# Optimization experiments

Measured on AMD Instinct MI355X. Metric: run time of the kernel, lower is better.

The kernel has to match this reference:

```python
import jax, jax.numpy as jnp
import numpy as np

KS = 32        # kernel_size (chunk size)
STRIDE = 16    # kernel_stride
H = 8          # head_num_k
D = 128        # head_dim
B = 4          # number of sequences
SEQ = 8192     # tokens per sequence (equal-length varlen batch)


def setup_inputs() -> dict:
    key = jax.random.key(0)
    k1, k2, k3, k4, k5 = jax.random.split(key, 5)
    kv = jax.random.normal(k1, (B * SEQ, 2, H, D), dtype=jnp.float32)
    cu_seqlens = jnp.arange(B + 1, dtype=jnp.int32) * SEQ
    # torch Conv1d default init: uniform(-s, s), s = 1/sqrt(in_channels*kernel_size)
    s = 1.0 / np.sqrt(D * KS)
    k_conv_w = jax.random.uniform(k2, (D, D, KS), jnp.float32, -s, s)
    k_conv_b = jax.random.uniform(k3, (D,), jnp.float32, -s, s)
    v_conv_w = jax.random.uniform(k4, (D, D, KS), jnp.float32, -s, s)
    v_conv_b = jax.random.uniform(k5, (D,), jnp.float32, -s, s)
    return {"kv": kv, "cu_seqlens": cu_seqlens,
            "k_conv_w": k_conv_w, "k_conv_b": k_conv_b,
            "v_conv_w": v_conv_w, "v_conv_b": v_conv_b}


def _chunk_indices(cu_seqlens, total_tokens):
    # Equal-length sequences: every strided chunk is valid, so shapes are static.
    batch = cu_seqlens.shape[0] - 1
    seqlen = total_tokens // batch
    nc = (seqlen - KS) // STRIDE + 1  # chunks per sequence
    starts = cu_seqlens[:-1].astype(jnp.int32)          # [B]
    offs = (jnp.arange(nc, dtype=jnp.int32) * STRIDE)   # [nc]
    pos = jnp.arange(KS, dtype=jnp.int32)               # [KS]
    idx = starts[:, None, None] + offs[None, :, None] + pos[None, None, :]  # [B, nc, KS]
    cu_comp = jnp.arange(batch + 1, dtype=jnp.int32) * nc
    return idx.reshape(batch * nc, KS), cu_comp


def reference(kv, cu_seqlens, k_conv_w, k_conv_b, v_conv_w, v_conv_b):
    idx, cu_comp = _chunk_indices(cu_seqlens, kv.shape[0])  # [L, KS]
    filtered = kv[idx.reshape(-1)].reshape(idx.shape[0], KS, 2, H, D)  # [L, KS, 2, H, D]
    k = filtered[:, :, 0]  # [L, KS, H, D]
    v = filtered[:, :, 1]
    # Conv1d with kernel spanning the whole chunk -> single output position:
    # out[l,h,o] = sum_{i,t} x[l,t,h,i] * W[o,i,t] + b[o]
    compress_k = jnp.einsum('lthi,oit->lho', k, k_conv_w) + k_conv_b
    compress_v = jnp.einsum('lthi,oit->lho', v, v_conv_w) + v_conv_b
    return compress_k, compress_v, cu_comp
```

## Files before the change

### kernel.cpp

```cpp
#include <hip/hip_runtime.h>

typedef __attribute__((ext_vector_type(8))) short bf16x8;
typedef __attribute__((ext_vector_type(4))) float f32x4;

#define MFMA16(A, B, C) __builtin_amdgcn_mfma_f32_16x16x32_bf16(A, B, C, 0, 0, 0)

__device__ __forceinline__ unsigned short f2bf(float f) {
  union { float f; unsigned int u; } v; v.f = f;
  return (unsigned short)((v.u + 0x7fffu + ((v.u >> 16) & 1u)) >> 16);
}
#define PK(LO, HI) (((unsigned int)f2bf(LO)) | ((unsigned int)f2bf(HI) << 16))

#define BAR() do {                                              \
    asm volatile("s_waitcnt lgkmcnt(0)" ::: "memory");          \
    __builtin_amdgcn_s_barrier();                               \
    asm volatile("" ::: "memory");                              \
  } while (0)

__global__ __launch_bounds__(256) void prep_kernel(
    const float* __restrict__ kw, const float* __restrict__ vw,
    unsigned short* __restrict__ imgK, unsigned short* __restrict__ imgV,
    int KSd,
    const int* __restrict__ cuin, float* __restrict__ outf,
    int cubase, int nb, int strideh) {
  __shared__ float wlds[128 * 33];
  int tid = threadIdx.x, bid = blockIdx.x;
  int sel = bid >> 7, o = bid & 127;
  int nel = 128 * KSd;
  int ksh = (KSd == 32) ? 5 : ((KSd == 16) ? 4 : 31 - __clz(KSd));
  int pad = KSd + 1;
  const float* wo = (sel ? vw : kw) + (size_t)o * nel;
  unsigned short* dst = sel ? imgV : imgK;
  for (int idx = tid; idx < nel; idx += 256) {
    int i = idx >> ksh, t = idx & (KSd - 1);
    wlds[i * pad + t] = wo[idx];
  }
  __syncthreads();
  int swE = (o & 7) << 3;
  for (int idx = tid; idx < nel; idx += 256) {
    int s = idx >> 6, c = idx & 63;
    int i = ((s & 1) << 6) + (c ^ swE);
    dst[((size_t)s << 13) + (o << 6) + c] = f2bf(wlds[i * pad + (s >> 1)]);
  }
  if (bid == 0 && tid <= nb) outf[cubase + tid] = (float)(cuin[tid] / strideh);
}

__global__ __launch_bounds__(512) void gemm_breg2_kernel(
    const float* __restrict__ kv,
    const float* __restrict__ biasK, const float* __restrict__ biasV,
    const unsigned short* __restrict__ imgK, const unsigned short* __restrict__ imgV,
    float* __restrict__ out,
    int vbase, int nc, int ltot, int tokmax, int seqb, int mtiles) {
  __shared__ __align__(16) unsigned short T[2][16640];
  int tid = threadIdx.x, bid = blockIdx.x;
  int per_sel = 8 * mtiles;
  int sel = (bid >= per_sel) ? 1 : 0;
  int rem = bid - sel * per_sel;
  int h = rem / mtiles, mtile = rem - h * mtiles;
  int m0 = mtile * 128;
  const unsigned short* img = sel ? imgV : imgK;
  const float* bias = sel ? biasV : biasK;
  int outbase = sel ? vbase : 0;
  int lane = tid & 63, wid = tid >> 6;
  int wm = wid >> 2, wn = wid & 3;
  int l15 = lane & 15, l4 = lane >> 4;

  int b0 = m0 / nc, c0 = m0 - b0 * nc;
  int btok0 = b0 * seqb + c0 * 16;
  int rb = nc - c0;

  int sjl = tid >> 4, sje = tid & 15;
  int soff = sel * 1024 + h * 128 + sje * 8;

  int kb0 = l4 * 16;
  int jbL[4], jswL[4], jbH[4], jswH[4];
#pragma unroll
  for (int mi = 0; mi < 4; ++mi) {
    int r = wm * 64 + mi * 16 + l15;
    int j = r + (r >= rb ? 1 : 0);
    jbL[mi] = j * 256;       jswL[mi] = (j & 7) << 4;
    jbH[mi] = (j + 1) * 256; jswH[mi] = ((j + 1) & 7) << 4;
  }

  int o0 = wn * 32 + l15, o1 = o0 + 16;
  int swE0 = (o0 & 7) << 3, swE1 = (o1 & 7) << 3;
  int ke = l4 * 8;
  int bo00 = o0 * 64 + ((ke) ^ swE0);
  int bo01 = o1 * 64 + ((ke) ^ swE1);
  int bo10 = o0 * 64 + ((32 + ke) ^ swE0);
  int bo11 = o1 * 64 + ((32 + ke) ^ swE1);

  f32x4 zz = {0.f, 0.f, 0.f, 0.f};
  f32x4 acc[4][2];
#pragma unroll
  for (int mi = 0; mi < 4; ++mi) { acc[mi][0] = zz; acc[mi][1] = zz; }

  float4 ta[5], tb[5];
  bf16x8 Bc0, Bc1, Bc2, Bc3, Bn0, Bn1, Bn2, Bn3;

#define STAGE_LOAD(P) do {                                                       \
    _Pragma("unroll")                                                            \
    for (int q_ = 0; q_ < 4; ++q_) {                                             \
      int t_ = btok0 + (q_ * 32 + sjl) * 16 + (P); if (t_ > tokmax) t_ = tokmax; \
      const float* a_ = kv + ((size_t)t_ << 11) + soff;                          \
      ta[q_] = *(const float4*)a_; tb[q_] = *(const float4*)(a_ + 4);            \
    }                                                                            \
    if (sjl < 2) {                                                               \
      int t_ = btok0 + (128 + sjl) * 16 + (P); if (t_ > tokmax) t_ = tokmax;     \
      const float* a_ = kv + ((size_t)t_ << 11) + soff;                          \
      ta[4] = *(const float4*)a_; tb[4] = *(const float4*)(a_ + 4);              \
    }                                                                            \
  } while (0)

#define T_WRITE(TB) do {                                                         \
    char* tp_ = (char*)(TB);                                                     \
    _Pragma("unroll")                                                            \
    for (int q_ = 0; q_ < 4; ++q_) {                                             \
      int js_ = q_ * 32 + sjl;                                                   \
      *(uint4*)(tp_ + js_ * 256 + ((sje * 16) ^ ((js_ & 7) << 4))) =             \
        make_uint4(PK(ta[q_].x, ta[q_].y), PK(ta[q_].z, ta[q_].w),               \
                   PK(tb[q_].x, tb[q_].y), PK(tb[q_].z, tb[q_].w));              \
    }                                                                            \
    if (sjl < 2) {                                                               \
      int js_ = 128 + sjl;                                                       \
      *(uint4*)(tp_ + js_ * 256 + ((sje * 16) ^ ((js_ & 7) << 4))) =             \
        make_uint4(PK(ta[4].x, ta[4].y), PK(ta[4].z, ta[4].w),                   \
                   PK(tb[4].x, tb[4].y), PK(tb[4].z, tb[4].w));                  \
    }                                                                            \
  } while (0)

#define B_LOADR(D0, D1, D2, D3, S) do {                                          \
    const unsigned short* bp_ = img + ((size_t)(S) << 13);                       \
    D0 = *(const bf16x8*)(bp_ + bo00);                                           \
    D1 = *(const bf16x8*)(bp_ + bo01);                                           \
    D2 = *(const bf16x8*)(bp_ + bo10);                                           \
    D3 = *(const bf16x8*)(bp_ + bo11);                                           \
  } while (0)

#define SUBSTEP(HF, JB, JSW, B00, B01, B10, B11) do {                            \
    const char* tc_ = (const char*)T[tcur];                                      \
    __builtin_amdgcn_s_setprio(1);                                               \
    {                                                                            \
      int kcA_ = (HF) * 128 + kb0;                                               \
      bf16x8 a_[4];                                                              \
      _Pragma("unroll")                                                          \
      for (int mi = 0; mi < 4; ++mi)                                             \
        a_[mi] = *(const bf16x8*)(tc_ + JB[mi] + (kcA_ ^ JSW[mi]));              \
      _Pragma("unroll")                                                          \
      for (int mi = 0; mi < 4; ++mi) {                                           \
        acc[mi][0] = MFMA16(a_[mi], B00, acc[mi][0]);                            \
        acc[mi][1] = MFMA16(a_[mi], B01, acc[mi][1]);                            \
      }                                                                          \
    }                                                                            \
    {                                                                            \
      int kcA_ = (HF) * 128 + 64 + kb0;                                          \
      bf16x8 a_[4];                                                              \
      _Pragma("unroll")                                                          \
      for (int mi = 0; mi < 4; ++mi)                                             \
        a_[mi] = *(const bf16x8*)(tc_ + JB[mi] + (kcA_ ^ JSW[mi]));              \
      _Pragma("unroll")                                                          \
      for (int mi = 0; mi < 4; ++mi) {                                           \
        acc[mi][0] = MFMA16(a_[mi], B10, acc[mi][0]);                            \
        acc[mi][1] = MFMA16(a_[mi], B11, acc[mi][1]);                            \
      }                                                                          \
    }                                                                            \
    __builtin_amdgcn_s_setprio(0);                                               \
  } while (0)

  int tcur = 0;
  STAGE_LOAD(0);
  T_WRITE(T[0]);
  B_LOADR(Bc0, Bc1, Bc2, Bc3, 0);
  B_LOADR(Bn0, Bn1, Bn2, Bn3, 1);
  BAR();

  for (int p = 0; p < 16; ++p) {
    if (p < 15) STAGE_LOAD(p + 1);
    SUBSTEP(0, jbL, jswL, Bc0, Bc1, Bc2, Bc3);
    B_LOADR(Bc0, Bc1, Bc2, Bc3, 2 * p + 32);
    SUBSTEP(1, jbL, jswL, Bn0, Bn1, Bn2, Bn3);
    B_LOADR(Bn0, Bn1, Bn2, Bn3, 2 * p + 33);
    SUBSTEP(0, jbH, jswH, Bc0, Bc1, Bc2, Bc3);
    if (p < 15) B_LOADR(Bc0, Bc1, Bc2, Bc3, 2 * p + 2);
    SUBSTEP(1, jbH, jswH, Bn0, Bn1, Bn2, Bn3);
    if (p < 15) {
      B_LOADR(Bn0, Bn1, Bn2, Bn3, 2 * p + 3);
      T_WRITE(T[tcur ^ 1]);
      BAR();
    }
    tcur ^= 1;
  }

#pragma unroll
  for (int ni = 0; ni < 2; ++ni) {
    int o_ = wn * 32 + ni * 16 + l15;
    float bv_ = bias[o_];
#pragma unroll
    for (int mi = 0; mi < 4; ++mi) {
      int lb_ = m0 + wm * 64 + mi * 16 + l4 * 4;
      f32x4 v_ = acc[mi][ni];
#pragma unroll
      for (int jj = 0; jj < 4; ++jj) {
        int ll_ = lb_ + jj;
        if (ll_ < ltot)
          out[(size_t)outbase + (size_t)ll_ * 1024 + h * 128 + o_] = v_[jj] + bv_;
      }
    }
  }
}

__global__ __launch_bounds__(512) void gemm_kernel(
    const float* __restrict__ kv,
    const float* __restrict__ biasK, const float* __restrict__ biasV,
    const unsigned short* __restrict__ imgK, const unsigned short* __restrict__ imgV,
    const float* __restrict__ kw, const float* __restrict__ vw,
    float* __restrict__ out,
    int selbase, int vbase, int nc, int ltot, int nsteps,
    int tokmax, int seqb, int strideh, int KSd, int mtiles) {
  __shared__ __align__(16) unsigned short As[2][4096];
  __shared__ __align__(16) unsigned short Bsf[2][8192];
  int tid = threadIdx.x, bid = blockIdx.x;
  int per_sel = 8 * mtiles;
  int sel = selbase + (bid >= per_sel);
  int rem = (bid >= per_sel) ? bid - per_sel : bid;
  int h = rem / mtiles, mtile = rem - h * mtiles;
  int m0 = mtile * 64;
  const unsigned short* img = sel ? imgV : imgK;
  const float* bias = sel ? biasV : biasK;
  const float* wsel = sel ? vw : kw;
  int outbase = sel ? vbase : 0;
  int lane = tid & 63, wid = tid >> 6;
  int warpM = wid >> 2, warpN = wid & 3;

  int aj = tid & 7, r = tid >> 3;
  int l = m0 + r; if (l > ltot - 1) l = ltot - 1;
  int b = l / nc, c = l - b * nc;
  int btok = b * seqb + c * strideh;
  const float* abase = kv + sel * 1024 + h * 128 + aj * 4;
  int swr = (r & 7) << 3;
  int awb0 = r * 128 + 2 * ((aj * 4) ^ swr);
  int awb1 = r * 128 + 2 * ((aj * 4 + 32) ^ swr);

  int o_g = tid >> 3, cb_g = (tid & 7) << 3;
  int ib_g = cb_g ^ ((o_g & 7) << 3);
  const float* g0 = wsel + (size_t)o_g * (KSd << 7);
  const float* g1 = g0 + ((size_t)64 * (KSd << 7));

  int kb0 = (lane >> 4) * 16;
  int arb[2], asw[2], brb[2], bsw[2];
#pragma unroll
  for (int mi = 0; mi < 2; ++mi) {
    int rr = warpM * 32 + mi * 16 + (lane & 15);
    arb[mi] = rr * 128; asw[mi] = (rr & 7) << 4;
  }
#pragma unroll
  for (int ni = 0; ni < 2; ++ni) {
    int oo = warpN * 32 + ni * 16 + (lane & 15);
    brb[ni] = oo * 128; bsw[ni] = (oo & 7) << 4;
  }

  f32x4 acc[2][2];
  f32x4 zz = {0.f, 0.f, 0.f, 0.f};
#pragma unroll
  for (int a = 0; a < 2; ++a)
#pragma unroll
    for (int b2 = 0; b2 < 2; ++b2) acc[a][b2] = zz;

  float4 Af0, Af1;
  uint4 Brr[2];

#define LOAD_STEP(S) do {                                                        \
    int tok_ = btok + ((S) >> 1); if (tok_ > tokmax) tok_ = tokmax;              \
    const float* ap_ = abase + ((size_t)tok_ << 11) + (((S) & 1) << 6);          \
    Af0 = *(const float4*)ap_;                                                   \
    Af1 = *(const float4*)(ap_ + 32);                                            \
    if (img) {                                                                   \
      const uint4* bsrc_ = (const uint4*)(img + ((size_t)(S) << 13));            \
      Brr[0] = bsrc_[tid];                                                       \
      Brr[1] = bsrc_[512 + tid];                                                 \
    } else {                                                                     \
      int t_ = (S) >> 1, i0_ = (((S) & 1) << 6) + ib_g;                          \
      unsigned int p0_[4], p1_[4];                                               \
      _Pragma("unroll")                                                          \
      for (int m = 0; m < 4; ++m) {                                              \
        p0_[m] = (unsigned int)f2bf(g0[(i0_ + 2*m) * KSd + t_])                  \
               | ((unsigned int)f2bf(g0[(i0_ + 2*m + 1) * KSd + t_]) << 16);     \
        p1_[m] = (unsigned int)f2bf(g1[(i0_ + 2*m) * KSd + t_])                  \
               | ((unsigned int)f2bf(g1[(i0_ + 2*m + 1) * KSd + t_]) << 16);     \
      }                                                                          \
      Brr[0] = make_uint4(p0_[0], p0_[1], p0_[2], p0_[3]);                       \
      Brr[1] = make_uint4(p1_[0], p1_[1], p1_[2], p1_[3]);                       \
    }                                                                            \
  } while (0)

#define WRITE_STEP(DB) do {                                                      \
    *(uint2*)((char*)As[DB] + awb0) = make_uint2(PK(Af0.x, Af0.y), PK(Af0.z, Af0.w)); \
    *(uint2*)((char*)As[DB] + awb1) = make_uint2(PK(Af1.x, Af1.y), PK(Af1.z, Af1.w)); \
    uint4* bdst_ = (uint4*)Bsf[DB];                                              \
    bdst_[tid] = Brr[0];                                                         \
    bdst_[512 + tid] = Brr[1];                                                   \
  } while (0)

#define COMPUTE_STEP(CB) do {                                                    \
    _Pragma("unroll")                                                            \
    for (int kk = 0; kk < 2; ++kk) {                                             \
      bf16x8 af_[2], bg_[2];                                                     \
      int kc_ = kk * 64 + kb0;                                                   \
      _Pragma("unroll")                                                          \
      for (int mi = 0; mi < 2; ++mi)                                             \
        af_[mi] = *(const bf16x8*)((const char*)As[CB] + arb[mi] + (kc_ ^ asw[mi])); \
      _Pragma("unroll")                                                          \
      for (int ni = 0; ni < 2; ++ni)                                             \
        bg_[ni] = *(const bf16x8*)((const char*)Bsf[CB] + brb[ni] + (kc_ ^ bsw[ni])); \
      _Pragma("unroll")                                                          \
      for (int mi = 0; mi < 2; ++mi)                                             \
      _Pragma("unroll")                                                          \
        for (int ni = 0; ni < 2; ++ni)                                           \
          acc[mi][ni] = MFMA16(af_[mi], bg_[ni], acc[mi][ni]);                   \
    }                                                                            \
  } while (0)

  LOAD_STEP(0);
  WRITE_STEP(0);
  __syncthreads();
  int cur = 0;
  for (int s = 0; s < nsteps; ++s) {
    if (s + 1 < nsteps) LOAD_STEP(s + 1);
    COMPUTE_STEP(cur);
    if (s + 1 < nsteps) WRITE_STEP(cur ^ 1);
    __syncthreads();
    cur ^= 1;
  }

  int l15 = lane & 15, l4 = lane >> 4;
#pragma unroll
  for (int ni = 0; ni < 2; ++ni) {
    int o = warpN * 32 + ni * 16 + l15;
    float bv = bias[o];
#pragma unroll
    for (int mi = 0; mi < 2; ++mi) {
      int lb = m0 + warpM * 32 + mi * 16 + l4 * 4;
      f32x4 v = acc[mi][ni];
#pragma unroll
      for (int jj = 0; jj < 4; ++jj) {
        int ll = lb + jj;
        if (ll < ltot)
          out[(size_t)outbase + (size_t)ll * 1024 + h * 128 + o] = v[jj] + bv;
      }
    }
  }
}

extern "C" void kernel_launch(void* const* d_in, const int* in_sizes, int n_in,
                              void* d_out, int out_size, void* d_ws, size_t ws_size,
                              hipStream_t stream) {
  long kvN = 0; int kvi = 0;
  for (int i = 0; i < n_in; ++i)
    if ((long)in_sizes[i] > kvN) { kvN = in_sizes[i]; kvi = i; }
  const float* kv = (const float*)d_in[kvi];
  const float *w0 = nullptr, *w1 = nullptr, *b0 = nullptr, *b1 = nullptr;
  const int* cuin = nullptr;
  int KSd = 32, nb = 4;
  for (int i = 0; i < n_in; ++i) {
    if (i == kvi) continue;
    int sz = in_sizes[i];
    if (sz == 128) { if (!b0) b0 = (const float*)d_in[i]; else if (!b1) b1 = (const float*)d_in[i]; }
    else if (sz <= 32) { nb = sz - 1; cuin = (const int*)d_in[i]; }
    else if (sz >= 4096) {
      if (!w0) { w0 = (const float*)d_in[i]; KSd = sz / 16384; }
      else if (!w1) w1 = (const float*)d_in[i];
    }
  }
  if (!w0) w0 = (const float*)d_in[2];
  if (!b0) b0 = (const float*)d_in[3];
  if (!w1) w1 = (const float*)d_in[4];
  if (!b1) b1 = (const float*)d_in[5];
  if (!cuin) cuin = (const int*)d_in[1];
  if (nb < 1) nb = 4;

  float* out = (float*)d_out;

  int cubase  = out_size - (nb + 1);
  int vbase   = cubase >> 1;
  int ltot    = cubase >> 11;
  int nc      = ltot / nb;
  int nsteps  = 2 * KSd;
  long tokens = kvN >> 11;
  int seqb    = (int)(tokens / nb);
  int strideh = (nc > 1) ? (seqb - KSd) / (nc - 1) : KSd;
  int tokmax  = (int)tokens - 1;
  int mtiles  = (ltot + 63) >> 6;
  int mt128   = (ltot + 127) >> 7;
  int per_sel = 8 * mtiles;

  size_t imgel = (size_t)nsteps * 8192;
  size_t imgbytes = imgel * 2;
  bool fast = (KSd == 32) && (strideh == 16) && (nc >= 128) &&
              (ws_size >= 2 * imgbytes);
  if (fast) {
    unsigned short* imgK = (unsigned short*)d_ws;
    unsigned short* imgV = imgK + imgel;
    prep_kernel<<<256, 256, 0, stream>>>(w0, w1, imgK, imgV, KSd,
                                         cuin, out, cubase, nb, strideh);
    gemm_breg2_kernel<<<2 * 8 * mt128, 512, 0, stream>>>(
        kv, b0, b1, imgK, imgV, out, vbase, nc, ltot, tokmax, seqb, mt128);
  } else if (ws_size >= 2 * imgbytes) {
    unsigned short* imgK = (unsigned short*)d_ws;
    unsigned short* imgV = imgK + imgel;
    prep_kernel<<<256, 256, 0, stream>>>(w0, w1, imgK, imgV, KSd,
                                         cuin, out, cubase, nb, strideh);
    gemm_kernel<<<2 * per_sel, 512, 0, stream>>>(kv, b0, b1, imgK, imgV, w0, w1, out,
        0, vbase, nc, ltot, nsteps, tokmax, seqb, strideh, KSd, mtiles);
  } else {
    prep_kernel<<<256, 256, 0, stream>>>(w0, w1, (unsigned short*)d_ws,
                                         (unsigned short*)d_ws, 0,
                                         cuin, out, cubase, nb, strideh);
    gemm_kernel<<<2 * per_sel, 512, 0, stream>>>(kv, b0, b1,
        (const unsigned short*)nullptr, (const unsigned short*)nullptr, w0, w1, out,
        0, vbase, nc, ltot, nsteps, tokmax, seqb, strideh, KSd, mtiles);
  }
}
```

Before: 79.64 us.

## Split K across warp pairs in fast GEMM and reduce partial sums via LDS

Changes the 8-warp layout from a 2x4 M-by-N grid to a 2x2 grid with two K-halves. Each warp now computes a 64x64 output tile over half of each K slice, so it reads fewer A fragments from LDS per MFMA. The two partial results are summed through shared memory before the bias add and store. This costs more accumulator registers (16 f32x4 instead of 8) and adds a reduction pass with an extra barrier at the end.

```diff
diff --git a/kernel.cpp b/kernel.cpp
--- a/kernel.cpp
+++ b/kernel.cpp
@@ -45,7 +45,7 @@
   if (bid == 0 && tid <= nb) outf[cubase + tid] = (float)(cuin[tid] / strideh);
 }
 
-__global__ __launch_bounds__(512) void gemm_breg2_kernel(
+__global__ __launch_bounds__(512) void gemm_ksplit_kernel(
     const float* __restrict__ kv,
     const float* __restrict__ biasK, const float* __restrict__ biasV,
     const unsigned short* __restrict__ imgK, const unsigned short* __restrict__ imgV,
@@ -62,7 +62,8 @@
   const float* bias = sel ? biasV : biasK;
   int outbase = sel ? vbase : 0;
   int lane = tid & 63, wid = tid >> 6;
-  int wm = wid >> 2, wn = wid & 3;
+  int kw = wid >> 2;
+  int wm = (wid >> 1) & 1, wn = wid & 1;
   int l15 = lane & 15, l4 = lane >> 4;
 
   int b0 = m0 / nc, c0 = m0 - b0 * nc;
@@ -72,7 +73,7 @@
   int sjl = tid >> 4, sje = tid & 15;
   int soff = sel * 1024 + h * 128 + sje * 8;
 
-  int kb0 = l4 * 16;
+  int kb0 = kw * 64 + l4 * 16;
   int jbL[4], jswL[4], jbH[4], jswH[4];
 #pragma unroll
   for (int mi = 0; mi < 4; ++mi) {
@@ -82,21 +83,22 @@
     jbH[mi] = (j + 1) * 256; jswH[mi] = ((j + 1) & 7) << 4;
   }
 
-  int o0 = wn * 32 + l15, o1 = o0 + 16;
-  int swE0 = (o0 & 7) << 3, swE1 = (o1 & 7) << 3;
-  int ke = l4 * 8;
-  int bo00 = o0 * 64 + ((ke) ^ swE0);
-  int bo01 = o1 * 64 + ((ke) ^ swE1);
-  int bo10 = o0 * 64 + ((32 + ke) ^ swE0);
-  int bo11 = o1 * 64 + ((32 + ke) ^ swE1);
+  int bo[4];
+#pragma unroll
+  for (int ni = 0; ni < 4; ++ni) {
+    int o_ = wn * 64 + ni * 16 + l15;
+    bo[ni] = o_ * 64 + ((kw * 32 + l4 * 8) ^ ((o_ & 7) << 3));
+  }
 
   f32x4 zz = {0.f, 0.f, 0.f, 0.f};
-  f32x4 acc[4][2];
-#pragma unroll
-  for (int mi = 0; mi < 4; ++mi) { acc[mi][0] = zz; acc[mi][1] = zz; }
+  f32x4 acc[4][4];
+#pragma unroll
+  for (int mi = 0; mi < 4; ++mi)
+#pragma unroll
+    for (int ni = 0; ni < 4; ++ni) acc[mi][ni] = zz;
 
   float4 ta[5], tb[5];
-  bf16x8 Bc0, Bc1, Bc2, Bc3, Bn0, Bn1, Bn2, Bn3;
+  bf16x8 Bc[4], Bn[4];
 
 #define STAGE_LOAD(P) do {                                                       \
     _Pragma("unroll")                                                            \
@@ -129,81 +131,80 @@
     }                                                                            \
   } while (0)
 
-#define B_LOADR(D0, D1, D2, D3, S) do {                                          \
+#define B_LOADR(DST, S) do {                                                     \
     const unsigned short* bp_ = img + ((size_t)(S) << 13);                       \
-    D0 = *(const bf16x8*)(bp_ + bo00);                                           \
-    D1 = *(const bf16x8*)(bp_ + bo01);                                           \
-    D2 = *(const bf16x8*)(bp_ + bo10);                                           \
-    D3 = *(const bf16x8*)(bp_ + bo11);                                           \
-  } while (0)
-
-#define SUBSTEP(HF, JB, JSW, B00, B01, B10, B11) do {                            \
+    _Pragma("unroll")                                                            \
+    for (int ni = 0; ni < 4; ++ni) DST[ni] = *(const bf16x8*)(bp_ + bo[ni]);     \
+  } while (0)
+
+#define SUBSTEP(HF, JB, JSW, BSET) do {                                          \
     const char* tc_ = (const char*)T[tcur];                                      \
     __builtin_amdgcn_s_setprio(1);                                               \
-    {                                                                            \
-      int kcA_ = (HF) * 128 + kb0;                                               \
-      bf16x8 a_[4];                                                              \
-      _Pragma("unroll")                                                          \
-      for (int mi = 0; mi < 4; ++mi)                                             \
-        a_[mi] = *(const bf16x8*)(tc_ + JB[mi] + (kcA_ ^ JSW[mi]));              \
-      _Pragma("unroll")                                                          \
-      for (int mi = 0; mi < 4; ++mi) {                                           \
-        acc[mi][0] = MFMA16(a_[mi], B00, acc[mi][0]);                            \
-        acc[mi][1] = MFMA16(a_[mi], B01, acc[mi][1]);                            \
-      }                                                                          \
-    }                                                                            \
-    {                                                                            \
-      int kcA_ = (HF) * 128 + 64 + kb0;                                          \
-      bf16x8 a_[4];                                                              \
-      _Pragma("unroll")                                                          \
-      for (int mi = 0; mi < 4; ++mi)                                             \
-        a_[mi] = *(const bf16x8*)(tc_ + JB[mi] + (kcA_ ^ JSW[mi]));              \
-      _Pragma("unroll")                                                          \
-      for (int mi = 0; mi < 4; ++mi) {                                           \
-        acc[mi][0] = MFMA16(a_[mi], B10, acc[mi][0]);                            \
-        acc[mi][1] = MFMA16(a_[mi], B11, acc[mi][1]);                            \
-      }                                                                          \
-    }                                                                            \
+    int kcA_ = (HF) * 128 + kb0;                                                 \
+    bf16x8 a_[4];                                                                \
+    _Pragma("unroll")                                                            \
+    for (int mi = 0; mi < 4; ++mi)                                               \
+      a_[mi] = *(const bf16x8*)(tc_ + JB[mi] + (kcA_ ^ JSW[mi]));                \
+    _Pragma("unroll")                                                            \
+    for (int mi = 0; mi < 4; ++mi)                                               \
+    _Pragma("unroll")                                                            \
+      for (int ni = 0; ni < 4; ++ni)                                             \
+        acc[mi][ni] = MFMA16(a_[mi], BSET[ni], acc[mi][ni]);                     \
     __builtin_amdgcn_s_setprio(0);                                               \
   } while (0)
 
   int tcur = 0;
   STAGE_LOAD(0);
   T_WRITE(T[0]);
-  B_LOADR(Bc0, Bc1, Bc2, Bc3, 0);
-  B_LOADR(Bn0, Bn1, Bn2, Bn3, 1);
+  B_LOADR(Bc, 0);
+  B_LOADR(Bn, 1);
   BAR();
 
   for (int p = 0; p < 16; ++p) {
     if (p < 15) STAGE_LOAD(p + 1);
-    SUBSTEP(0, jbL, jswL, Bc0, Bc1, Bc2, Bc3);
-    B_LOADR(Bc0, Bc1, Bc2, Bc3, 2 * p + 32);
-    SUBSTEP(1, jbL, jswL, Bn0, Bn1, Bn2, Bn3);
-    B_LOADR(Bn0, Bn1, Bn2, Bn3, 2 * p + 33);
-    SUBSTEP(0, jbH, jswH, Bc0, Bc1, Bc2, Bc3);
-    if (p < 15) B_LOADR(Bc0, Bc1, Bc2, Bc3, 2 * p + 2);
-    SUBSTEP(1, jbH, jswH, Bn0, Bn1, Bn2, Bn3);
+    SUBSTEP(0, jbL, jswL, Bc);
+    B_LOADR(Bc, 2 * p + 32);
+    SUBSTEP(1, jbL, jswL, Bn);
+    B_LOADR(Bn, 2 * p + 33);
+    SUBSTEP(0, jbH, jswH, Bc);
+    if (p < 15) B_LOADR(Bc, 2 * p + 2);
+    SUBSTEP(1, jbH, jswH, Bn);
     if (p < 15) {
-      B_LOADR(Bn0, Bn1, Bn2, Bn3, 2 * p + 3);
+      B_LOADR(Bn, 2 * p + 3);
       T_WRITE(T[tcur ^ 1]);
       BAR();
     }
     tcur ^= 1;
   }
 
-#pragma unroll
-  for (int ni = 0; ni < 2; ++ni) {
-    int o_ = wn * 32 + ni * 16 + l15;
-    float bv_ = bias[o_];
-#pragma unroll
-    for (int mi = 0; mi < 4; ++mi) {
-      int lb_ = m0 + wm * 64 + mi * 16 + l4 * 4;
-      f32x4 v_ = acc[mi][ni];
-#pragma unroll
-      for (int jj = 0; jj < 4; ++jj) {
-        int ll_ = lb_ + jj;
-        if (ll_ < ltot)
-          out[(size_t)outbase + (size_t)ll_ * 1024 + h * 128 + o_] = v_[jj] + bv_;
+  BAR();
+  float* red = (float*)T;
+  int widx = wm * 2 + wn;
+  if (kw == 1) {
+#pragma unroll
+    for (int mi = 0; mi < 4; ++mi)
+#pragma unroll
+      for (int ni = 0; ni < 4; ++ni)
+        *(f32x4*)(red + (size_t)(((widx * 16 + mi * 4 + ni) * 64 + lane)) * 4) = acc[mi][ni];
+  }
+  BAR();
+  if (kw == 0) {
+#pragma unroll
+    for (int ni = 0; ni < 4; ++ni) {
+      int o_ = wn * 64 + ni * 16 + l15;
+      float bv_ = bias[o_];
+#pragma unroll
+      for (int mi = 0; mi < 4; ++mi) {
+        f32x4 other = *(const f32x4*)(red + (size_t)(((widx * 16 + mi * 4 + ni) * 64 + lane)) * 4);
+        f32x4 v_ = acc[mi][ni];
+        int lb_ = m0 + wm * 64 + mi * 16 + l4 * 4;
+#pragma unroll
+        for (int jj = 0; jj < 4; ++jj) {
+          int ll_ = lb_ + jj;
+          if (ll_ < ltot)
+            out[(size_t)outbase + (size_t)ll_ * 1024 + h * 128 + o_] =
+                v_[jj] + other[jj] + bv_;
+        }
       }
     }
   }
@@ -402,7 +403,7 @@
     unsigned short* imgV = imgK + imgel;
     prep_kernel<<<256, 256, 0, stream>>>(w0, w1, imgK, imgV, KSd,
                                          cuin, out, cubase, nb, strideh);
-    gemm_breg2_kernel<<<2 * 8 * mt128, 512, 0, stream>>>(
+    gemm_ksplit_kernel<<<2 * 8 * mt128, 512, 0, stream>>>(
         kv, b0, b1, imgK, imgV, out, vbase, nc, ltot, tokmax, seqb, mt128);
   } else if (ws_size >= 2 * imgbytes) {
     unsigned short* imgK = (unsigned short*)d_ws;
```

After: 83.13 us. +4.4%, slower.
